# Performance work log

Hardware: AMD Instinct MI355X
Metric: run time of the kernel (lower is better)

The kernel has to match this reference:

```python
import jax, jax.numpy as jnp
import numpy as np

N, D, H, E, L = 4096, 512, 8, 131072, 2
DH = D // H  # per-head dim


def _layernorm(x, g, b, eps=1e-5):
    mu = x.mean(-1, keepdims=True)
    v = ((x - mu) ** 2).mean(-1, keepdims=True)
    return (x - mu) * jax.lax.rsqrt(v + eps) * g + b


def setup_inputs() -> dict:
    key = jax.random.key(0)
    ks = jax.random.split(key, 8)
    s = np.float32(1.0 / np.sqrt(D))
    return {
        "x": jax.random.normal(ks[0], (N, D), jnp.float32),
        "edge_index": jax.random.randint(ks[1], (2, E), 0, N),
        "edge_attr": jax.random.normal(ks[2], (E, 16), jnp.float32),
        "W_gcn": jax.random.normal(ks[3], (L, D, D), jnp.float32) * s,
        "ln1_g": jnp.ones((L, D), jnp.float32),
        "ln1_b": jnp.zeros((L, D), jnp.float32),
        "Wq": jax.random.normal(ks[4], (L, D, D), jnp.float32) * s,
        "bq": jnp.zeros((L, D), jnp.float32),
        "Wk": jax.random.normal(ks[5], (L, D, D), jnp.float32) * s,
        "bk": jnp.zeros((L, D), jnp.float32),
        "Wv": jax.random.normal(ks[6], (L, D, D), jnp.float32) * s,
        "bv": jnp.zeros((L, D), jnp.float32),
        "Wo": jax.random.normal(ks[7], (L, D, D), jnp.float32) * s,
        "bo": jnp.zeros((L, D), jnp.float32),
        "ln2_g": jnp.ones((L, D), jnp.float32),
        "ln2_b": jnp.zeros((L, D), jnp.float32),
    }


def reference(x, edge_index, edge_attr, W_gcn, ln1_g, ln1_b, Wq, bq, Wk, bk, Wv, bv, Wo, bo, ln2_g, ln2_b):
    src, dst = edge_index[0], edge_index[1]
    # symmetric GCN normalization (add_self_loops=False): deg from scattering 1s at target
    deg = jax.ops.segment_sum(jnp.ones(src.shape[0], x.dtype), dst, num_segments=N)
    dinv = jnp.where(deg > 0, jax.lax.rsqrt(jnp.maximum(deg, 1e-12)), 0.0)
    enorm = (dinv[src] * dinv[dst])[:, None]  # [E,1]
    scale = 1.0 / np.sqrt(D)  # MHA scale = 1/sqrt(D_x), applied to BOTH Q and K
    for i in range(L):
        # GCNConv (no bias): gather - linear - scatter-sum
        h = x @ W_gcn[i]
        h = jax.ops.segment_sum(h[src] * enorm, dst, num_segments=N)
        # PairNorm (scale=1, scale_individually=False)
        c = h - h.mean(0, keepdims=True)
        h = c * jax.lax.rsqrt(1e-5 + (c * c).sum(-1).mean())
        # residual: relu(x) + x
        h = jax.nn.relu(h) + h
        # LayerNorm 1
        h = _layernorm(h, ln1_g[i], ln1_b[i])
        # MultiHeadAttentionBlock (self-attn, B=1) -- faithful raw reshapes of original
        Q = (h @ Wq[i].T + bq[i]) * scale            # [N,D]
        K = (h @ Wk[i].T + bk[i]) * scale            # [N,D]
        V = h @ Wv[i].T + bv[i]                      # [N,D]
        Qr = Q.reshape(H, DH, N).transpose(0, 2, 1)  # view(B*H,d,L).transpose(1,2)
        Kr = K.reshape(H, DH, N)                     # view(B*H,d,L)
        w = jax.nn.softmax(jnp.einsum('hld,hdm->hlm', Qr, Kr), axis=-1)  # [H,N,N]
        Vr = V.reshape(H, DH, N).transpose(0, 2, 1)  # [H,N,d]
        a = jnp.einsum('hlm,hmd->hld', w, Vr).reshape(N, D)
        h = a @ Wo[i].T + bo[i]
        # LayerNorm 2
        x = _layernorm(h, ln2_g[i], ln2_b[i])
    return x
```

## Files before the change

kernel.cpp:

```cpp
#include <hip/hip_runtime.h>


#define NN 4096
#define DD 512
#define HH 8
#define DH 64
#define EE 131072

typedef float f32x2 __attribute__((ext_vector_type(2)));
typedef float f32x4 __attribute__((ext_vector_type(4)));
typedef short short8 __attribute__((ext_vector_type(8)));
typedef unsigned short u16x4 __attribute__((ext_vector_type(4)));
typedef __bf16 bf16x8 __attribute__((ext_vector_type(8)));

static __device__ __forceinline__ unsigned short f2bf(float f) {
  return __builtin_bit_cast(unsigned short, (__bf16)f);
}
static __device__ __forceinline__ float bf2f(unsigned short s) {
  return __uint_as_float(((unsigned)s) << 16);
}

static __device__ __forceinline__ f32x4 mfma16(short8 a, short8 b, f32x4 c) {
  return __builtin_amdgcn_mfma_f32_16x16x32_bf16(
      __builtin_bit_cast(bf16x8, a), __builtin_bit_cast(bf16x8, b), c, 0, 0, 0);
}

static __device__ __forceinline__ void gload16(const unsigned short* g, unsigned short* l) {
  __builtin_amdgcn_global_load_lds((const __attribute__((address_space(1))) unsigned int*)g,
                                   (__attribute__((address_space(3))) unsigned int*)l, 16, 0, 0);
}

__global__ __launch_bounds__(256) void deg_k(const int* __restrict__ ei, float* __restrict__ deg) {
  int t = blockIdx.x * 256 + threadIdx.x;
  atomicAdd(&deg[ei[EE + t]], 1.0f);
}

__global__ __launch_bounds__(256) void dinv_k(const float* __restrict__ deg, float* __restrict__ dinv) {
  int t = blockIdx.x * 256 + threadIdx.x;
  float dg = deg[t];
  dinv[t] = dg > 0.f ? rsqrtf(fmaxf(dg, 1e-12f)) : 0.f;
}

__global__ __launch_bounds__(256) void scan_k(const float* __restrict__ deg,
                                              int* __restrict__ rowstart,
                                              int* __restrict__ cursor) {
  __shared__ int part[256];
  const int t = threadIdx.x;
  int loc[16];
  int s = 0;
#pragma unroll
  for (int j = 0; j < 16; ++j) {
    loc[j] = s;
    s += (int)deg[t * 16 + j];
  }
  part[t] = s;
  __syncthreads();
  for (int off = 1; off < 256; off <<= 1) {
    int v = (t >= off) ? part[t - off] : 0;
    __syncthreads();
    part[t] += v;
    __syncthreads();
  }
  int base = (t > 0) ? part[t - 1] : 0;
#pragma unroll
  for (int j = 0; j < 16; ++j) {
    int rs = base + loc[j];
    rowstart[t * 16 + j] = rs;
    cursor[t * 16 + j] = rs;
  }
  if (t == 255) rowstart[4096] = part[255];
}

__global__ __launch_bounds__(256) void csr_fill_k(const int* __restrict__ ei,
                                                  const float* __restrict__ dinv,
                                                  int* __restrict__ cursor,
                                                  int* __restrict__ ecol,
                                                  float* __restrict__ ewt) {
  int e = blockIdx.x * 256 + threadIdx.x;
  int s = ei[e], d = ei[EE + e];
  int pos = atomicAdd(&cursor[d], 1);
  ecol[pos] = s;
  ewt[pos] = dinv[s] * dinv[d];
}

__global__ __launch_bounds__(256) void cvt_k(const float* __restrict__ s,
                                             unsigned short* __restrict__ d, int n4) {
  int i = blockIdx.x * 256 + threadIdx.x;
  if (i < n4) {
    f32x4 v = *(const f32x4*)&s[i * 4];
    u16x4 o;
#pragma unroll
    for (int j = 0; j < 4; ++j) o[j] = f2bf(v[j]);
    *(u16x4*)&d[i * 4] = o;
  }
}

struct P8 { const float* p[8]; };
__global__ __launch_bounds__(256) void cvt8_k(P8 s, unsigned short* __restrict__ d) {
  const int which = blockIdx.y;
  const float* src = s.p[which];
  unsigned short* dst = d + (size_t)which * 262144;
  int i = blockIdx.x * 256 + threadIdx.x;
  f32x4 v = *(const f32x4*)&src[i * 4];
  u16x4 o;
#pragma unroll
  for (int j = 0; j < 4; ++j) o[j] = f2bf(v[j]);
  *(u16x4*)&dst[i * 4] = o;
}

__global__ __launch_bounds__(256) void wtr2_k(const float* __restrict__ in,
                                              unsigned short* __restrict__ out) {
  __shared__ unsigned short sm[64][72];
  const int z = blockIdx.z;
  const float* inz = in + (size_t)z * DD * DD;
  unsigned short* outz = out + (size_t)z * 262144;
  const int k0 = blockIdx.y * 64, j0 = blockIdx.x * 64;
  const int t = threadIdx.x;
  const int r = t >> 2, q = (t & 3) * 16;
  const float* src = inz + (size_t)(k0 + r) * 512 + j0 + q;
#pragma unroll
  for (int jj = 0; jj < 16; ++jj) sm[r][q + jj] = f2bf(src[jj]);
  __syncthreads();
  short8 s0, s1;
#pragma unroll
  for (int j = 0; j < 8; ++j) {
    s0[j] = (short)sm[q + j][r];
    s1[j] = (short)sm[q + 8 + j][r];
  }
  *(short8*)&outz[(size_t)(j0 + r) * 512 + k0 + q] = s0;
  *(short8*)&outz[(size_t)(j0 + r) * 512 + k0 + q + 8] = s1;
}

__global__ __launch_bounds__(256) void gather_k(const unsigned short* __restrict__ hb,
                                                const int* __restrict__ rowstart,
                                                const int* __restrict__ ecol,
                                                const float* __restrict__ ewt,
                                                float* __restrict__ h1) {
  __shared__ int s_col[256];
  __shared__ float s_w[256];
  const int node = blockIdx.x, t = threadIdx.x;
  const int beg = rowstart[node], end = rowstart[node + 1];
  float a0 = 0.f, a1 = 0.f;
  for (int base = beg; base < end; base += 256) {
    int n = min(256, end - base);
    __syncthreads();
    if (t < n) {
      s_col[t] = ecol[base + t];
      s_w[t] = ewt[base + t];
    }
    __syncthreads();
    for (int j = 0; j < n; ++j) {
      int s = s_col[j];
      float en = s_w[j];
      unsigned v = *(const unsigned*)&hb[(size_t)s * DD + 2 * t];
      a0 += en * __uint_as_float(v << 16);
      a1 += en * __uint_as_float(v & 0xFFFF0000u);
    }
  }
  f32x2 acc = {a0, a1};
  *(f32x2*)&h1[(size_t)node * DD + 2 * t] = acc;
}

template <bool HAS_BIAS, bool OUT_BF16>
__global__ __launch_bounds__(256) void gemm_bt_k(const unsigned short* __restrict__ A,
                                                 const unsigned short* __restrict__ B,
                                                 const float* __restrict__ bias, float scale,
                                                 void* __restrict__ Cv, int M, int Nc, int K) {
  __shared__ __align__(16) unsigned short a_sm[2][64][64];
  __shared__ __align__(16) unsigned short b_sm[2][64][64];
  const int tid = threadIdx.x, w = tid >> 6, lane = tid & 63;
  const int g = lane >> 4, c16 = lane & 15;
  const int n0 = blockIdx.x * 64, m0 = blockIdx.y * 64;
  const int wm = (w >> 1) * 32, wn = (w & 1) * 32;
  const int srow = lane >> 3, cg = lane & 7;
  const int swz = ((cg * 16) ^ (srow << 4)) >> 1;
  const unsigned short* ag = A + (size_t)(m0 + w * 8 + srow) * K + swz;
  const unsigned short* bg = B + (size_t)(n0 + w * 8 + srow) * K + swz;
  f32x4 acc[2][2] = {};

  gload16(ag, &a_sm[0][w * 8][0]);
  gload16(ag + (size_t)32 * K, &a_sm[0][w * 8 + 32][0]);
  gload16(bg, &b_sm[0][w * 8][0]);
  gload16(bg + (size_t)32 * K, &b_sm[0][w * 8 + 32][0]);
  __syncthreads();

  const int rx = (c16 & 7) << 4;
  const int NK = K >> 6;
  for (int ks = 0; ks < NK; ++ks) {
    const int cb = ks & 1;
    if (ks < NK - 1) {
      const size_t ko = (size_t)(ks + 1) * 64;
      gload16(ag + ko, &a_sm[cb ^ 1][w * 8][0]);
      gload16(ag + ko + (size_t)32 * K, &a_sm[cb ^ 1][w * 8 + 32][0]);
      gload16(bg + ko, &b_sm[cb ^ 1][w * 8][0]);
      gload16(bg + ko + (size_t)32 * K, &b_sm[cb ^ 1][w * 8 + 32][0]);
    }
#pragma unroll
    for (int kc = 0; kc < 2; ++kc) {
      const int co = (kc * 64 + g * 16) ^ rx;
      short8 af0 = *(const short8*)((const char*)&a_sm[cb][wm + c16][0] + co);
      short8 af1 = *(const short8*)((const char*)&a_sm[cb][wm + 16 + c16][0] + co);
      short8 bf0 = *(const short8*)((const char*)&b_sm[cb][wn + c16][0] + co);
      short8 bf1 = *(const short8*)((const char*)&b_sm[cb][wn + 16 + c16][0] + co);
      acc[0][0] = mfma16(af0, bf0, acc[0][0]);
      acc[0][1] = mfma16(af0, bf1, acc[0][1]);
      acc[1][0] = mfma16(af1, bf0, acc[1][0]);
      acc[1][1] = mfma16(af1, bf1, acc[1][1]);
    }
    __syncthreads();
  }
#pragma unroll
  for (int fm = 0; fm < 2; ++fm)
#pragma unroll
    for (int fn = 0; fn < 2; ++fn)
#pragma unroll
      for (int r = 0; r < 4; ++r) {
        int row = m0 + wm + fm * 16 + g * 4 + r;
        int col = n0 + wn + fn * 16 + c16;
        float v = acc[fm][fn][r];
        if (HAS_BIAS) v += bias[col];
        v *= scale;
        if (OUT_BF16)
          ((unsigned short*)Cv)[(size_t)row * Nc + col] = f2bf(v);
        else
          ((float*)Cv)[(size_t)row * Nc + col] = v;
      }
}

__global__ __launch_bounds__(256) void colstat_k(const float* __restrict__ hin,
                                                 float* __restrict__ colsum,
                                                 float* __restrict__ sumsq) {
  const int t = threadIdx.x;
  const int r0 = blockIdx.x * 32;
  float a0 = 0.f, a1 = 0.f, sq = 0.f;
  for (int r = 0; r < 32; ++r) {
    float v0 = hin[(size_t)(r0 + r) * DD + t];
    float v1 = hin[(size_t)(r0 + r) * DD + 256 + t];
    a0 += v0; a1 += v1;
    sq += v0 * v0 + v1 * v1;
  }
  atomicAdd(&colsum[t], a0);
  atomicAdd(&colsum[t + 256], a1);
#pragma unroll
  for (int m = 1; m <= 32; m <<= 1) sq += __shfl_xor(sq, m);
  __shared__ float rr[4];
  int w = t >> 6, lane = t & 63;
  if (lane == 0) rr[w] = sq;
  __syncthreads();
  if (t == 0) atomicAdd(sumsq, rr[0] + rr[1] + rr[2] + rr[3]);
}

__global__ __launch_bounds__(256) void finalize_pn_k(const float* __restrict__ colsum,
                                                     const float* __restrict__ sumsq,
                                                     float* __restrict__ mu,
                                                     float* __restrict__ rnp) {
  const int t = threadIdx.x;
  float m0 = colsum[t] * (1.f / (float)NN);
  float m1 = colsum[t + 256] * (1.f / (float)NN);
  mu[t] = m0;
  mu[t + 256] = m1;
  float sq = m0 * m0 + m1 * m1;
#pragma unroll
  for (int m = 1; m <= 32; m <<= 1) sq += __shfl_xor(sq, m);
  __shared__ float rr[4];
  int w = t >> 6, lane = t & 63;
  if (lane == 0) rr[w] = sq;
  __syncthreads();
  if (t == 0) {
    float musq = rr[0] + rr[1] + rr[2] + rr[3];
    *rnp = rsqrtf(1e-5f + (*sumsq) * (1.f / (float)NN) - musq);
  }
}

template <bool PN, bool WF32>
__global__ __launch_bounds__(256) void rowfuse_k(const float* __restrict__ hin,
                                                 const float* __restrict__ mu,
                                                 const float* __restrict__ rnp,
                                                 const float* __restrict__ gg,
                                                 const float* __restrict__ bb,
                                                 float* __restrict__ outf,
                                                 unsigned short* __restrict__ outb) {
  const int row = blockIdx.x, t = threadIdx.x;
  const size_t base = (size_t)row * DD;
  f32x2 vv = *(const f32x2*)&hin[base + 2 * t];
  float v0 = vv[0], v1 = vv[1];
  if (PN) {
    float rn = *rnp;
    v0 = (v0 - mu[2 * t]) * rn;
    v1 = (v1 - mu[2 * t + 1]) * rn;
    v0 = fmaxf(v0, 0.f) + v0;
    v1 = fmaxf(v1, 0.f) + v1;
  }
  float s1 = v0 + v1, s2 = v0 * v0 + v1 * v1;
#pragma unroll
  for (int m = 1; m <= 32; m <<= 1) {
    s1 += __shfl_xor(s1, m);
    s2 += __shfl_xor(s2, m);
  }
  __shared__ float r1[4], r2[4];
  int w = t >> 6, lane = t & 63;
  if (lane == 0) { r1[w] = s1; r2[w] = s2; }
  __syncthreads();
  s1 = r1[0] + r1[1] + r1[2] + r1[3];
  s2 = r2[0] + r2[1] + r2[2] + r2[3];
  float mean = s1 * (1.f / (float)DD);
  float var = s2 * (1.f / (float)DD) - mean * mean;
  float inv = rsqrtf(var + 1e-5f);
  float y0 = (v0 - mean) * inv * gg[2 * t] + bb[2 * t];
  float y1 = (v1 - mean) * inv * gg[2 * t + 1] + bb[2 * t + 1];
  if (WF32) {
    f32x2 yo = {y0, y1};
    *(f32x2*)&outf[base + 2 * t] = yo;
  }
  *(unsigned*)&outb[base + 2 * t] = (unsigned)f2bf(y0) | ((unsigned)f2bf(y1) << 16);
}

__global__ __launch_bounds__(256) void transpose2_pk(const unsigned short* __restrict__ in0,
                                                     const unsigned short* __restrict__ in1,
                                                     unsigned short* __restrict__ out0,
                                                     unsigned short* __restrict__ out1) {
  __shared__ __align__(16) unsigned short sm[64][72];
  const unsigned short* in = blockIdx.z ? in1 : in0;
  unsigned short* out = blockIdx.z ? out1 : out0;
  const int m0 = blockIdx.x * 64, p0 = blockIdx.y * 64;
  const int t = threadIdx.x;
  const int r = t >> 2, q = (t & 3) * 16;
  *(short8*)&sm[r][q] = *(const short8*)&in[(size_t)(p0 + r) * NN + m0 + q];
  *(short8*)&sm[r][q + 8] = *(const short8*)&in[(size_t)(p0 + r) * NN + m0 + q + 8];
  __syncthreads();
  short8 s0, s1;
#pragma unroll
  for (int j = 0; j < 8; ++j) {
    s0[j] = (short)sm[q + j][r];
    s1[j] = (short)sm[q + 8 + j][r];
  }
  *(short8*)&out[(size_t)(m0 + r) * DD + p0 + q] = s0;
  *(short8*)&out[(size_t)(m0 + r) * DD + p0 + q + 8] = s1;
}

__global__ __launch_bounds__(256, 4) void attn_k(const unsigned short* __restrict__ Qt,
                                                 const unsigned short* __restrict__ Kt,
                                                 const unsigned short* __restrict__ Vb,
                                                 unsigned short* __restrict__ Op0,
                                                 unsigned short* __restrict__ Op1,
                                                 float* __restrict__ ms) {
  __shared__ __align__(16) unsigned short k_sm[2][64][64];
  __shared__ __align__(16) unsigned short v_sm[2][64][64];
  __shared__ __align__(16) unsigned short p_sm[4][16][64];
  const int tid = threadIdx.x, w = tid >> 6, lane = tid & 63;
  const int g = lane >> 4, c16 = lane & 15;
  const int h = blockIdx.y, z = blockIdx.z;
  const int zbase = z * (NN / 2);
  const int l0 = blockIdx.x * 64 + w * 16;
  unsigned short* __restrict__ Op = z ? Op1 : Op0;

  short8 qf0 = *(const short8*)&Qt[(size_t)(l0 + c16) * DD + h * 64 + g * 8];
  short8 qf1 = *(const short8*)&Qt[(size_t)(l0 + c16) * DD + h * 64 + 32 + g * 8];

  const int srow = lane >> 3, cg = lane & 7;
  const int swz = ((cg * 16) ^ (srow << 4)) >> 1;
  const unsigned short* kgbase = Kt + (size_t)(zbase + w * 16 + srow) * DD + h * 64 + swz;
  const unsigned short* vgbase = Vb + (size_t)(h * 64 + w * 16 + srow) * NN + zbase + swz;

  gload16(kgbase, &k_sm[0][w * 16][0]);
  gload16(kgbase + (size_t)8 * DD, &k_sm[0][w * 16 + 8][0]);
  gload16(vgbase, &v_sm[0][w * 16][0]);
  gload16(vgbase + (size_t)8 * NN, &v_sm[0][w * 16 + 8][0]);
  __syncthreads();

  float M = 0.f;
  f32x4 sacc = {};
  f32x4 oacc[4] = {};
  const int sx = (c16 & 7) << 4;
  short8 ones8;
#pragma unroll
  for (int j = 0; j < 8; ++j) ones8[j] = (short)0x3F80;

  for (int t = 0; t < 32; ++t) {
    const int cb = t & 1;
    if (t < 31) {
      const size_t ko = (size_t)(t + 1) * 64 * DD;
      gload16(kgbase + ko, &k_sm[cb ^ 1][w * 16][0]);
      gload16(kgbase + ko + (size_t)8 * DD, &k_sm[cb ^ 1][w * 16 + 8][0]);
      gload16(vgbase + (t + 1) * 64, &v_sm[cb ^ 1][w * 16][0]);
      gload16(vgbase + (t + 1) * 64 + (size_t)8 * NN, &v_sm[cb ^ 1][w * 16 + 8][0]);
    }
    f32x4 sf[4] = {};
#pragma unroll
    for (int fn = 0; fn < 4; ++fn) {
      const char* kr = (const char*)&k_sm[cb][fn * 16 + c16][0];
      short8 b0 = *(const short8*)(kr + ((g * 16) ^ sx));
      short8 b1 = *(const short8*)(kr + ((64 + g * 16) ^ sx));
      sf[fn] = mfma16(qf0, b0, sf[fn]);
      sf[fn] = mfma16(qf1, b1, sf[fn]);
    }
    float a0 = fmaxf(fmaxf(sf[0][0], sf[0][1]), fmaxf(sf[0][2], sf[0][3]));
    float a1 = fmaxf(fmaxf(sf[1][0], sf[1][1]), fmaxf(sf[1][2], sf[1][3]));
    float a2 = fmaxf(fmaxf(sf[2][0], sf[2][1]), fmaxf(sf[2][2], sf[2][3]));
    float a3 = fmaxf(fmaxf(sf[3][0], sf[3][1]), fmaxf(sf[3][2], sf[3][3]));
    float amax = fmaxf(fmaxf(a0, a1), fmaxf(a2, a3));
    if (__any(amax > M + 25.f)) {
      float wmax = amax;
#pragma unroll
      for (int m = 1; m <= 32; m <<= 1) wmax = fmaxf(wmax, __shfl_xor(wmax, m));
      float alpha = __expf(M - wmax);
#pragma unroll
      for (int r = 0; r < 4; ++r) sacc[r] *= alpha;
#pragma unroll
      for (int fd = 0; fd < 4; ++fd)
#pragma unroll
        for (int r = 0; r < 4; ++r) oacc[fd][r] *= alpha;
      M = wmax;
    }
#pragma unroll
    for (int fn = 0; fn < 4; ++fn)
#pragma unroll
      for (int r = 0; r < 4; ++r) sf[fn][r] = __expf(sf[fn][r] - M);
#pragma unroll
    for (int fn = 0; fn < 4; ++fn)
#pragma unroll
      for (int r = 0; r < 4; ++r) {
        const int prow = g * 4 + r;
        const int pb = ((fn * 16 + c16) * 2) ^ ((prow & 7) << 4);
        *(unsigned short*)((char*)&p_sm[w][prow][0] + pb) = f2bf(sf[fn][r]);
      }
#pragma unroll
    for (int kk = 0; kk < 2; ++kk) {
      const int rb = (kk * 64 + g * 16) ^ ((c16 & 7) << 4);
      short8 pa = *(const short8*)((const char*)&p_sm[w][c16][0] + rb);
      sacc = mfma16(pa, ones8, sacc);
#pragma unroll
      for (int fd = 0; fd < 4; ++fd) {
        const char* vr = (const char*)&v_sm[cb][fd * 16 + c16][0];
        short8 vbf = *(const short8*)(vr + ((kk * 64 + g * 16) ^ sx));
        oacc[fd] = mfma16(pa, vbf, oacc[fd]);
      }
    }
    __syncthreads();
  }
#pragma unroll
  for (int fd = 0; fd < 4; ++fd)
#pragma unroll
    for (int r = 0; r < 4; ++r) {
      int l = l0 + g * 4 + r;
      Op[((size_t)h * NN + l) * DH + fd * 16 + c16] = f2bf(oacc[fd][r]);
    }
  if (c16 == 0) {
#pragma unroll
    for (int r = 0; r < 4; ++r) {
      int hl = h * NN + l0 + g * 4 + r;
      f32x2 pr = {M, sacc[r]};
      *(f32x2*)&ms[((size_t)z * (HH * NN) + hl) * 2] = pr;
    }
  }
}

__global__ __launch_bounds__(256) void attn_merge_k(const unsigned short* __restrict__ Op0,
                                                    const unsigned short* __restrict__ Op1,
                                                    const float* __restrict__ ms,
                                                    unsigned short* __restrict__ Out) {
  const int t = threadIdx.x;
  const int hl = blockIdx.x * 4 + (t >> 6);
  const int d = t & 63;
  float M0 = ms[(size_t)hl * 2], s0 = ms[(size_t)hl * 2 + 1];
  float M1 = ms[((size_t)(HH * NN) + hl) * 2], s1 = ms[((size_t)(HH * NN) + hl) * 2 + 1];
  float M = fmaxf(M0, M1);
  float w0 = __expf(M0 - M), w1 = __expf(M1 - M);
  float inv = 1.f / (w0 * s0 + w1 * s1);
  size_t idx = (size_t)hl * DH + d;
  Out[idx] = f2bf((w0 * bf2f(Op0[idx]) + w1 * bf2f(Op1[idx])) * inv);
}

extern "C" void kernel_launch(void* const* d_in, const int* in_sizes, int n_in,
                              void* d_out, int out_size, void* d_ws, size_t ws_size,
                              hipStream_t stream) {
  const float* x = (const float*)d_in[0];
  const int* ei = (const int*)d_in[1];
  const float* Wg = (const float*)d_in[3];
  const float* ln1g = (const float*)d_in[4];
  const float* ln1b = (const float*)d_in[5];
  const float* Wq = (const float*)d_in[6];
  const float* bq = (const float*)d_in[7];
  const float* Wk = (const float*)d_in[8];
  const float* bk = (const float*)d_in[9];
  const float* Wv = (const float*)d_in[10];
  const float* bv = (const float*)d_in[11];
  const float* Wo = (const float*)d_in[12];
  const float* bo = (const float*)d_in[13];
  const float* ln2g = (const float*)d_in[14];
  const float* ln2b = (const float*)d_in[15];
  float* out = (float*)d_out;

  char* p = (char*)d_ws;
  float* deg = (float*)p;
  float* dinv = deg + 4096;
  float* colsum = deg + 8192;
  float* sumsq = deg + 8704;
  float* mu = deg + 8768;
  float* rnp = deg + 9280;
  float* h1 = deg + 16384;
  unsigned short* xb = (unsigned short*)(h1 + (1u << 21));
  unsigned short* actb = xb + (1u << 21);
  unsigned short* h4b = actb + (1u << 21);
  unsigned short* proj = h4b + (1u << 21);
  unsigned short* Vb = proj + (1u << 21);
  unsigned short* Qt = Vb + (1u << 21);
  unsigned short* Kt = Qt + (1u << 21);
  unsigned short* wb = Kt + (1u << 21);
  float* msbuf = (float*)(wb + 10u * 262144);
  int* rowstart = (int*)(msbuf + 131072);
  int* cursor = rowstart + 4104;
  int* ecol = cursor + 4096;
  float* ewt = (float*)(ecol + EE);
  const size_t needed = (size_t)((char*)(ewt + EE) - (char*)d_ws);
  if (ws_size < needed) return;

  unsigned short* Op0b = (unsigned short*)h1;
  unsigned short* Op1b = h4b;

  const float SCALE = 0.044194173824159216f;
  const size_t WS = (size_t)DD * DD;

  hipMemsetAsync(deg, 0, 4096 * sizeof(float), stream);
  deg_k<<<EE / 256, 256, 0, stream>>>(ei, deg);
  dinv_k<<<NN / 256, 256, 0, stream>>>(deg, dinv);
  scan_k<<<1, 256, 0, stream>>>(deg, rowstart, cursor);
  csr_fill_k<<<EE / 256, 256, 0, stream>>>(ei, dinv, cursor, ecol, ewt);

  cvt_k<<<2048, 256, 0, stream>>>(x, xb, 524288);
  wtr2_k<<<dim3(8, 8, 2), 256, 0, stream>>>(Wg, wb);
  P8 s8;
  s8.p[0] = Wq; s8.p[1] = Wq + WS;
  s8.p[2] = Wk; s8.p[3] = Wk + WS;
  s8.p[4] = Wv; s8.p[5] = Wv + WS;
  s8.p[6] = Wo; s8.p[7] = Wo + WS;
  cvt8_k<<<dim3(256, 8), 256, 0, stream>>>(s8, wb + 2u * 262144);

  const dim3 gg(8, 64);
  for (int i = 0; i < 2; ++i) {
    gemm_bt_k<false, true><<<gg, 256, 0, stream>>>(
        xb, wb + (0 + i) * 262144, nullptr, 1.f, actb, NN, DD, DD);
    gather_k<<<NN, 256, 0, stream>>>(actb, rowstart, ecol, ewt, h1);
    hipMemsetAsync(colsum, 0, 513 * sizeof(float), stream);
    colstat_k<<<128, 256, 0, stream>>>(h1, colsum, sumsq);
    finalize_pn_k<<<1, 256, 0, stream>>>(colsum, sumsq, mu, rnp);
    rowfuse_k<true, false><<<NN, 256, 0, stream>>>(h1, mu, rnp, ln1g + i * DD, ln1b + i * DD,
                                                   nullptr, h4b);
    gemm_bt_k<true, true><<<gg, 256, 0, stream>>>(
        h4b, wb + (2 + i) * 262144, bq + i * DD, SCALE, proj, NN, DD, DD);
    gemm_bt_k<true, true><<<gg, 256, 0, stream>>>(
        h4b, wb + (4 + i) * 262144, bk + i * DD, SCALE, actb, NN, DD, DD);
    gemm_bt_k<true, true><<<gg, 256, 0, stream>>>(
        h4b, wb + (6 + i) * 262144, bv + i * DD, 1.f, Vb, NN, DD, DD);
    transpose2_pk<<<dim3(64, 8, 2), 256, 0, stream>>>(proj, actb, Qt, Kt);
    attn_k<<<dim3(64, 8, 2), 256, 0, stream>>>(Qt, Kt, Vb, Op0b, Op1b, msbuf);
    attn_merge_k<<<HH * NN / 4, 256, 0, stream>>>(Op0b, Op1b, msbuf, actb);
    gemm_bt_k<true, false><<<gg, 256, 0, stream>>>(
        actb, wb + (8 + i) * 262144, bo + i * DD, 1.f, h1, NN, DD, DD);
    rowfuse_k<false, true><<<NN, 256, 0, stream>>>(h1, nullptr, nullptr, ln2g + i * DD,
                                                   ln2b + i * DD, out, xb);
  }
}
```

Measured before the change: 432.3 us.

## Fuse QKV projections, remap attention blocks per XCD, use exp2 softmax, unroll gather

The three Q/K/V GEMMs become one launch over a 24x64 grid, and each block picks its weight, bias, scale and output from its column index. Q is pre-scaled by log2(e) so the attention and merge kernels can use exp2f instead of __expf, and the rescale threshold is adjusted to match. Attention blocks are reindexed over a flat grid so that each head/half pair stays on one XCD, which should improve L2 reuse of K and V. The gather loop is unrolled by four with two accumulator pairs, and colsum zeroing moves into the gather kernel, dropping one memset. The exp2 change slightly alters rounding, and the XCD mapping assumes round-robin block dispatch across 8 XCDs.

```diff
diff --git a/kernel.cpp b/kernel.cpp
--- a/kernel.cpp
+++ b/kernel.cpp
@@ -12,6 +12,9 @@
 typedef short short8 __attribute__((ext_vector_type(8)));
 typedef unsigned short u16x4 __attribute__((ext_vector_type(4)));
 typedef __bf16 bf16x8 __attribute__((ext_vector_type(8)));
+
+#define SCALE_K 0.044194173824159216f
+#define SCALE_Q 0.06375872343889103f
 
 static __device__ __forceinline__ unsigned short f2bf(float f) {
   return __builtin_bit_cast(unsigned short, (__bf16)f);
@@ -135,12 +138,18 @@
                                                 const int* __restrict__ rowstart,
                                                 const int* __restrict__ ecol,
                                                 const float* __restrict__ ewt,
-                                                float* __restrict__ h1) {
+                                                float* __restrict__ h1,
+                                                float* __restrict__ colsum) {
   __shared__ int s_col[256];
   __shared__ float s_w[256];
   const int node = blockIdx.x, t = threadIdx.x;
+  if (node == 0) {
+    colsum[t] = 0.f;
+    colsum[t + 256] = 0.f;
+    if (t == 0) colsum[512] = 0.f;
+  }
   const int beg = rowstart[node], end = rowstart[node + 1];
-  float a0 = 0.f, a1 = 0.f;
+  float a0 = 0.f, a1 = 0.f, b0 = 0.f, b1 = 0.f;
   for (int base = beg; base < end; base += 256) {
     int n = min(256, end - base);
     __syncthreads();
@@ -149,15 +158,32 @@
       s_w[t] = ewt[base + t];
     }
     __syncthreads();
-    for (int j = 0; j < n; ++j) {
-      int s = s_col[j];
+    int j = 0;
+    for (; j + 3 < n; j += 4) {
+      int c0 = s_col[j], c1 = s_col[j + 1], c2 = s_col[j + 2], c3 = s_col[j + 3];
+      float e0 = s_w[j], e1 = s_w[j + 1], e2 = s_w[j + 2], e3 = s_w[j + 3];
+      unsigned v0 = *(const unsigned*)&hb[(size_t)c0 * DD + 2 * t];
+      unsigned v1 = *(const unsigned*)&hb[(size_t)c1 * DD + 2 * t];
+      unsigned v2 = *(const unsigned*)&hb[(size_t)c2 * DD + 2 * t];
+      unsigned v3 = *(const unsigned*)&hb[(size_t)c3 * DD + 2 * t];
+      a0 += e0 * __uint_as_float(v0 << 16);
+      a1 += e0 * __uint_as_float(v0 & 0xFFFF0000u);
+      b0 += e1 * __uint_as_float(v1 << 16);
+      b1 += e1 * __uint_as_float(v1 & 0xFFFF0000u);
+      a0 += e2 * __uint_as_float(v2 << 16);
+      a1 += e2 * __uint_as_float(v2 & 0xFFFF0000u);
+      b0 += e3 * __uint_as_float(v3 << 16);
+      b1 += e3 * __uint_as_float(v3 & 0xFFFF0000u);
+    }
+    for (; j < n; ++j) {
+      int c = s_col[j];
       float en = s_w[j];
-      unsigned v = *(const unsigned*)&hb[(size_t)s * DD + 2 * t];
+      unsigned v = *(const unsigned*)&hb[(size_t)c * DD + 2 * t];
       a0 += en * __uint_as_float(v << 16);
       a1 += en * __uint_as_float(v & 0xFFFF0000u);
     }
   }
-  f32x2 acc = {a0, a1};
+  f32x2 acc = {a0 + b0, a1 + b1};
   *(f32x2*)&h1[(size_t)node * DD + 2 * t] = acc;
 }
 
@@ -224,6 +250,78 @@
           ((unsigned short*)Cv)[(size_t)row * Nc + col] = f2bf(v);
         else
           ((float*)Cv)[(size_t)row * Nc + col] = v;
+      }
+}
+
+__global__ __launch_bounds__(256) void gemm_qkv_k(const unsigned short* __restrict__ A,
+                                                  const unsigned short* __restrict__ wbase,
+                                                  const float* __restrict__ bq,
+                                                  const float* __restrict__ bk,
+                                                  const float* __restrict__ bv,
+                                                  unsigned short* __restrict__ Qo,
+                                                  unsigned short* __restrict__ Ko,
+                                                  unsigned short* __restrict__ Vo,
+                                                  int layer) {
+  __shared__ __align__(16) unsigned short a_sm[2][64][64];
+  __shared__ __align__(16) unsigned short b_sm[2][64][64];
+  const int tid = threadIdx.x, w = tid >> 6, lane = tid & 63;
+  const int g = lane >> 4, c16 = lane & 15;
+  const int n0g = blockIdx.x * 64, m0 = blockIdx.y * 64;
+  const int which = n0g >> 9;
+  const int n0 = n0g & 511;
+  const unsigned short* B = wbase + (size_t)(which * 2 + layer) * 262144;
+  const float* bias = which == 0 ? bq : (which == 1 ? bk : bv);
+  const float scale = which == 0 ? SCALE_Q : (which == 1 ? SCALE_K : 1.f);
+  unsigned short* dst = which == 0 ? Qo : (which == 1 ? Ko : Vo);
+  const int K = DD;
+  const int wm = (w >> 1) * 32, wn = (w & 1) * 32;
+  const int srow = lane >> 3, cg = lane & 7;
+  const int swz = ((cg * 16) ^ (srow << 4)) >> 1;
+  const unsigned short* ag = A + (size_t)(m0 + w * 8 + srow) * K + swz;
+  const unsigned short* bg = B + (size_t)(n0 + w * 8 + srow) * K + swz;
+  f32x4 acc[2][2] = {};
+
+  gload16(ag, &a_sm[0][w * 8][0]);
+  gload16(ag + (size_t)32 * K, &a_sm[0][w * 8 + 32][0]);
+  gload16(bg, &b_sm[0][w * 8][0]);
+  gload16(bg + (size_t)32 * K, &b_sm[0][w * 8 + 32][0]);
+  __syncthreads();
+
+  const int rx = (c16 & 7) << 4;
+  const int NK = K >> 6;
+  for (int ks = 0; ks < NK; ++ks) {
+    const int cb = ks & 1;
+    if (ks < NK - 1) {
+      const size_t ko = (size_t)(ks + 1) * 64;
+      gload16(ag + ko, &a_sm[cb ^ 1][w * 8][0]);
+      gload16(ag + ko + (size_t)32 * K, &a_sm[cb ^ 1][w * 8 + 32][0]);
+      gload16(bg + ko, &b_sm[cb ^ 1][w * 8][0]);
+      gload16(bg + ko + (size_t)32 * K, &b_sm[cb ^ 1][w * 8 + 32][0]);
+    }
+#pragma unroll
+    for (int kc = 0; kc < 2; ++kc) {
+      const int co = (kc * 64 + g * 16) ^ rx;
+      short8 af0 = *(const short8*)((const char*)&a_sm[cb][wm + c16][0] + co);
+      short8 af1 = *(const short8*)((const char*)&a_sm[cb][wm + 16 + c16][0] + co);
+      short8 bf0 = *(const short8*)((const char*)&b_sm[cb][wn + c16][0] + co);
+      short8 bf1 = *(const short8*)((const char*)&b_sm[cb][wn + 16 + c16][0] + co);
+      acc[0][0] = mfma16(af0, bf0, acc[0][0]);
+      acc[0][1] = mfma16(af0, bf1, acc[0][1]);
+      acc[1][0] = mfma16(af1, bf0, acc[1][0]);
+      acc[1][1] = mfma16(af1, bf1, acc[1][1]);
+    }
+    __syncthreads();
+  }
+#pragma unroll
+  for (int fm = 0; fm < 2; ++fm)
+#pragma unroll
+    for (int fn = 0; fn < 2; ++fn)
+#pragma unroll
+      for (int r = 0; r < 4; ++r) {
+        int row = m0 + wm + fm * 16 + g * 4 + r;
+        int col = n0 + wn + fn * 16 + c16;
+        float v = (acc[fm][fn][r] + bias[col]) * scale;
+        dst[(size_t)row * DD + col] = f2bf(v);
       }
 }
 
@@ -349,9 +447,12 @@
   __shared__ __align__(16) unsigned short p_sm[4][16][64];
   const int tid = threadIdx.x, w = tid >> 6, lane = tid & 63;
   const int g = lane >> 4, c16 = lane & 15;
-  const int h = blockIdx.y, z = blockIdx.z;
+  const int L = blockIdx.x;
+  const int xcd = L & 7, slot = L >> 3;
+  const int c = xcd + 8 * (slot >> 6);
+  const int h = c >> 1, z = c & 1;
   const int zbase = z * (NN / 2);
-  const int l0 = blockIdx.x * 64 + w * 16;
+  const int l0 = (slot & 63) * 64 + w * 16;
   unsigned short* __restrict__ Op = z ? Op1 : Op0;
 
   short8 qf0 = *(const short8*)&Qt[(size_t)(l0 + c16) * DD + h * 64 + g * 8];
@@ -399,11 +500,11 @@
     float a2 = fmaxf(fmaxf(sf[2][0], sf[2][1]), fmaxf(sf[2][2], sf[2][3]));
     float a3 = fmaxf(fmaxf(sf[3][0], sf[3][1]), fmaxf(sf[3][2], sf[3][3]));
     float amax = fmaxf(fmaxf(a0, a1), fmaxf(a2, a3));
-    if (__any(amax > M + 25.f)) {
+    if (__any(amax > M + 36.1f)) {
       float wmax = amax;
 #pragma unroll
       for (int m = 1; m <= 32; m <<= 1) wmax = fmaxf(wmax, __shfl_xor(wmax, m));
-      float alpha = __expf(M - wmax);
+      float alpha = exp2f(M - wmax);
 #pragma unroll
       for (int r = 0; r < 4; ++r) sacc[r] *= alpha;
 #pragma unroll
@@ -415,7 +516,7 @@
 #pragma unroll
     for (int fn = 0; fn < 4; ++fn)
 #pragma unroll
-      for (int r = 0; r < 4; ++r) sf[fn][r] = __expf(sf[fn][r] - M);
+      for (int r = 0; r < 4; ++r) sf[fn][r] = exp2f(sf[fn][r] - M);
 #pragma unroll
     for (int fn = 0; fn < 4; ++fn)
 #pragma unroll
@@ -465,7 +566,7 @@
   float M0 = ms[(size_t)hl * 2], s0 = ms[(size_t)hl * 2 + 1];
   float M1 = ms[((size_t)(HH * NN) + hl) * 2], s1 = ms[((size_t)(HH * NN) + hl) * 2 + 1];
   float M = fmaxf(M0, M1);
-  float w0 = __expf(M0 - M), w1 = __expf(M1 - M);
+  float w0 = exp2f(M0 - M), w1 = exp2f(M1 - M);
   float inv = 1.f / (w0 * s0 + w1 * s1);
   size_t idx = (size_t)hl * DH + d;
   Out[idx] = f2bf((w0 * bf2f(Op0[idx]) + w1 * bf2f(Op1[idx])) * inv);
@@ -518,7 +619,6 @@
   unsigned short* Op0b = (unsigned short*)h1;
   unsigned short* Op1b = h4b;
 
-  const float SCALE = 0.044194173824159216f;
   const size_t WS = (size_t)DD * DD;
 
   hipMemsetAsync(deg, 0, 4096 * sizeof(float), stream);
@@ -540,20 +640,15 @@
   for (int i = 0; i < 2; ++i) {
     gemm_bt_k<false, true><<<gg, 256, 0, stream>>>(
         xb, wb + (0 + i) * 262144, nullptr, 1.f, actb, NN, DD, DD);
-    gather_k<<<NN, 256, 0, stream>>>(actb, rowstart, ecol, ewt, h1);
-    hipMemsetAsync(colsum, 0, 513 * sizeof(float), stream);
+    gather_k<<<NN, 256, 0, stream>>>(actb, rowstart, ecol, ewt, h1, colsum);
     colstat_k<<<128, 256, 0, stream>>>(h1, colsum, sumsq);
     finalize_pn_k<<<1, 256, 0, stream>>>(colsum, sumsq, mu, rnp);
     rowfuse_k<true, false><<<NN, 256, 0, stream>>>(h1, mu, rnp, ln1g + i * DD, ln1b + i * DD,
                                                    nullptr, h4b);
-    gemm_bt_k<true, true><<<gg, 256, 0, stream>>>(
-        h4b, wb + (2 + i) * 262144, bq + i * DD, SCALE, proj, NN, DD, DD);
-    gemm_bt_k<true, true><<<gg, 256, 0, stream>>>(
-        h4b, wb + (4 + i) * 262144, bk + i * DD, SCALE, actb, NN, DD, DD);
-    gemm_bt_k<true, true><<<gg, 256, 0, stream>>>(
-        h4b, wb + (6 + i) * 262144, bv + i * DD, 1.f, Vb, NN, DD, DD);
+    gemm_qkv_k<<<dim3(24, 64), 256, 0, stream>>>(
+        h4b, wb + 2u * 262144, bq + i * DD, bk + i * DD, bv + i * DD, proj, actb, Vb, i);
     transpose2_pk<<<dim3(64, 8, 2), 256, 0, stream>>>(proj, actb, Qt, Kt);
-    attn_k<<<dim3(64, 8, 2), 256, 0, stream>>>(Qt, Kt, Vb, Op0b, Op1b, msbuf);
+    attn_k<<<1024, 256, 0, stream>>>(Qt, Kt, Vb, Op0b, Op1b, msbuf);
     attn_merge_k<<<HH * NN / 4, 256, 0, stream>>>(Op0b, Op1b, msbuf, actb);
     gemm_bt_k<true, false><<<gg, 256, 0, stream>>>(
         actb, wb + (8 + i) * 262144, bo + i * DD, 1.f, h1, NN, DD, DD);
```

Measured after the change: 430.7 us. Within noise of the previous version (-0.4%).
